# Optimization experiments

Hardware: AMD Instinct MI355X
Metric: run time of the kernel (lower is better)

The kernel has to match this reference:

```python
import jax, jax.numpy as jnp
import numpy as np

B, BS, M, D = 64, 8, 512, 256  # b = bs * neg_sample_num, neg_sample_num = 8
NEG_FILL = -1e10


def setup_inputs() -> dict:
    key = jax.random.key(0)
    ks = jax.random.split(key, 7)
    x = jax.random.normal(ks[0], (B, M, D), jnp.float32)
    y = jax.random.normal(ks[1], (BS, M, D), jnp.float32)
    mask_x = jax.random.randint(ks[2], (B, M), 0, 2).astype(bool).at[:, 0].set(True)
    mask_y = jax.random.randint(ks[3], (BS, M), 0, 2).astype(bool).at[:, 0].set(True)
    scale = 1.0 / np.sqrt(D)
    Wq = jax.random.normal(ks[4], (D, D), jnp.float32) * scale  # torch Linear weight [out,in]
    Wk = jax.random.normal(ks[5], (D, D), jnp.float32) * scale
    Wv = jax.random.normal(ks[6], (D, D), jnp.float32) * scale
    return {"x": x, "y": y, "mask_x": mask_x, "mask_y": mask_y, "Wq": Wq, "Wk": Wk, "Wv": Wv}


def reference(x, y, mask_x, mask_y, Wq, Wk, Wv):
    # Projections (torch Linear: x @ W.T, no bias)
    Qx, Kx, Vx = x @ Wq.T, x @ Wk.T, x @ Wv.T
    Qy, Ky, Vy = y @ Wq.T, y @ Wk.T, y @ Wv.T
    b, m, d = Qx.shape
    bs = Ky.shape[0]
    neg = b // bs  # neg_sample_num branch (bs != b)

    scores_x = jnp.einsum('bid,bjd->bij', Qx, Kx)   # [b,m,m]
    scores_y = jnp.einsum('bid,bjd->bij', Qy, Ky)   # [bs,m,m]
    # Q_x grouped as [bs, neg, m, d] then transposed to [neg, bs, m, d];
    # K_y is tiled over neg (pure broadcast), so contract directly against [bs,m,d].
    Qx_e = Qx.reshape(bs, neg, m, d).swapaxes(0, 1)  # [neg,bs,m,d]
    scores_xy = jnp.einsum('nsid,sjd->nsij', Qx_e, Ky)  # [neg,bs,m,m]

    mx = mask_x[:, :, None]  # [b,m,1]
    my = mask_y[:, :, None]  # [bs,m,1]
    scores_x = jnp.where(mx & mx.swapaxes(1, 2), scores_x, NEG_FILL)
    scores_y = jnp.where(my & my.swapaxes(1, 2), scores_y, NEG_FILL)

    mask_xy = mask_x.reshape(bs, neg, m, 1).swapaxes(0, 1) & mask_y[None, :, None, :]  # [neg,bs,m,m]
    scores_xy = jnp.where(mask_xy, scores_xy, NEG_FILL)

    # y_len[n, s] = sum(mask_y[s]) for every n (repeat/view/sum/transpose in torch)
    y_len = jnp.broadcast_to(jnp.sum(mask_y.astype(jnp.int32), axis=1)[None, :], (neg, bs))

    probs_x = jax.nn.softmax(scores_x, axis=-1)
    probs_y = jax.nn.softmax(scores_y, axis=-1)
    probs_xy = jax.nn.softmax(scores_xy, axis=-1)

    ctx_x = jnp.einsum('bij,bjd->bid', probs_x, Vx)
    ctx_y = jnp.einsum('bij,bjd->bid', probs_y, Vy)
    return (ctx_x, ctx_y, scores_x, scores_y, probs_xy, mask_xy, y_len)
```

## Files before the change

### kernel.cpp

```cpp
#include <hip/hip_runtime.h>
#include <cstdint>

#define NEG_FILL_F (-10000000000.0f)
constexpr int BB     = 64;
constexpr int BS_    = 8;
constexpr int MM     = 512;
constexpr int DD     = 256;
constexpr int ROWS_X = BB * MM;
constexpr int ROWS_Y = BS_ * MM;
constexpr int ROWS_ALL = ROWS_X + ROWS_Y;
constexpr int KS     = 512;

typedef __attribute__((ext_vector_type(8))) short short8;
typedef __attribute__((ext_vector_type(4))) float f32x4;

__device__ inline unsigned short rne_bf16(float f) {
    unsigned int u = __float_as_uint(f);
    u = (u + 0x7FFFu + ((u >> 16) & 1u)) >> 16;
    return (unsigned short)u;
}
__device__ inline float bf2f(unsigned short h) {
    return __uint_as_float(((unsigned int)h) << 16);
}

__device__ inline f32x4 mfma16(short8 a, short8 b, f32x4 c) {
    return __builtin_amdgcn_mfma_f32_16x16x32_bf16(a, b, c, 0, 0, 0);
}

__device__ inline void gld16(const unsigned short* g, unsigned short* l) {
    __builtin_amdgcn_global_load_lds(
        (const __attribute__((address_space(1))) unsigned int*)g,
        (__attribute__((address_space(3))) unsigned int*)l, 16, 0, 0);
}

__device__ inline void mfma_4x4(const short8 af[4], const short8 bf_[4],
                                f32x4 acc[4][4]) {
    #pragma unroll
    for (int i = 0; i < 4; ++i)
        #pragma unroll
        for (int j = 0; j < 4; ++j)
            acc[i][j] = mfma16(af[i], bf_[j], acc[i][j]);
}

__device__ inline int awin32(int w) { return (((w >> 3) == 1) ? 256 : 0) + (w & 7) * 32; }
__device__ inline int bwin32(int w) { return (((w >> 3) == 2) ? 256 : 0) + (w & 7) * 32; }

__device__ inline void stage32(unsigned short* dstbase,
                               const unsigned short* __restrict__ src,
                               int srccol, int wave, int lane)
{
    #pragma unroll
    for (int s4 = 0; s4 < 2; ++s4) {
        const int c   = s4 * 256 + wave * 64 + lane;
        const int r   = c >> 2;
        const int cin = (c & 3) ^ (r & 3);
        gld16(src + (size_t)r * KS + srccol + cin * 8,
              dstbase + (size_t)(s4 * 256 + wave * 64) * 8);
    }
}

__device__ inline void frag4_x32(const unsigned short (*T)[32], int rbase,
                                 int lid, int quad, short8 f[4])
{
    const int q = quad ^ (lid & 3);
    #pragma unroll
    for (int i = 0; i < 4; ++i)
        f[i] = *(const short8*)&T[rbase + i * 16 + lid][q * 8];
}

__global__ __launch_bounds__(256) void convw_kernel(
    const float* __restrict__ Wq, const float* __restrict__ Wk,
    const float* __restrict__ Wv, unsigned short* __restrict__ Wb)
{
    const int g  = blockIdx.x * 256 + threadIdx.x;
    const int e  = g * 8;
    const int zi = e >> 16;
    const int off = e & 65535;
    const int row = off >> 8, k0 = off & 255;
    const float* W = (zi == 0) ? Wq : (zi == 1 ? Wk : Wv);
    float4 v0 = *(const float4*)(W + off);
    float4 v1 = *(const float4*)(W + off + 4);
    const float fv[8] = {v0.x, v0.y, v0.z, v0.w, v1.x, v1.y, v1.z, v1.w};
    short8 hh, ll;
    #pragma unroll
    for (int i = 0; i < 8; ++i) {
        unsigned short h = rne_bf16(fv[i]);
        hh[i] = (short)h;
        ll[i] = (short)rne_bf16(fv[i] - bf2f(h));
    }
    unsigned short* dst = Wb + (size_t)zi * 131072 + (size_t)row * KS;
    *(short8*)(dst + k0)       = hh;
    *(short8*)(dst + 256 + k0) = ll;
}

__global__ __launch_bounds__(256) void convx_kernel(
    const float* __restrict__ x, const float* __restrict__ y,
    unsigned short* __restrict__ xs)
{
    const int g   = blockIdx.x * 256 + threadIdx.x;
    const int row = g >> 5;
    const int off = (g & 31) * 8;
    const float* src = (row < ROWS_X) ? (x + (size_t)row * DD)
                                      : (y + (size_t)(row - ROWS_X) * DD);
    float4 v0 = *(const float4*)(src + off);
    float4 v1 = *(const float4*)(src + off + 4);
    const float fv[8] = {v0.x, v0.y, v0.z, v0.w, v1.x, v1.y, v1.z, v1.w};
    short8 hh, ll;
    #pragma unroll
    for (int i = 0; i < 8; ++i) {
        unsigned short h = rne_bf16(fv[i]);
        hh[i] = (short)h;
        ll[i] = (short)rne_bf16(fv[i] - bf2f(h));
    }
    unsigned short* dst = xs + (size_t)row * KS;
    *(short8*)(dst + off)       = hh;
    *(short8*)(dst + 256 + off) = ll;
}

__global__ __launch_bounds__(256) void proj_kernel(
    const unsigned short* __restrict__ xs,
    const unsigned short* __restrict__ Wb,
    unsigned short* __restrict__ Qa, unsigned short* __restrict__ Kb,
    unsigned short* __restrict__ Vt)
{
    const int xcd = blockIdx.x & 7, idx = blockIdx.x >> 3;
    const int lin = xcd * 216 + idx;
    const int bx  = lin / 6;
    const int rem = lin - bx * 6;
    const int z    = rem >> 1;
    const int row0 = bx * 128;
    const int col0 = (rem & 1) * 128;
    const unsigned short* Asrc = xs + (size_t)row0 * KS;
    const unsigned short* Bsrc = Wb + (size_t)z * 131072 + (size_t)col0 * KS;

    __shared__ unsigned short Ab[2][128][32];
    __shared__ unsigned short Bb[2][128][32];

    const int t = threadIdx.x;
    const int wave = t >> 6, lane = t & 63, quad = lane >> 4, lid = lane & 15;
    const int wrow = (wave & 1) * 64, wcol = (wave >> 1) * 64;

    f32x4 acc[4][4];
    #pragma unroll
    for (int i = 0; i < 4; ++i)
        #pragma unroll
        for (int j = 0; j < 4; ++j) acc[i][j] = (f32x4){0.f, 0.f, 0.f, 0.f};

    stage32(&Ab[0][0][0], Asrc, awin32(0), wave, lane);
    stage32(&Bb[0][0][0], Bsrc, bwin32(0), wave, lane);
    __syncthreads();
    int cur = 0;
    for (int w = 0; w < 23; ++w) {
        stage32(&Ab[cur ^ 1][0][0], Asrc, awin32(w + 1), wave, lane);
        stage32(&Bb[cur ^ 1][0][0], Bsrc, bwin32(w + 1), wave, lane);
        short8 af[4], bf_[4];
        frag4_x32(Ab[cur], wrow, lid, quad, af);
        frag4_x32(Bb[cur], wcol, lid, quad, bf_);
        mfma_4x4(af, bf_, acc);
        __syncthreads();
        cur ^= 1;
    }
    {
        short8 af[4], bf_[4];
        frag4_x32(Ab[cur], wrow, lid, quad, af);
        frag4_x32(Bb[cur], wcol, lid, quad, bf_);
        mfma_4x4(af, bf_, acc);
    }

    if (z == 2) {
        #pragma unroll
        for (int i = 0; i < 4; ++i) {
            const int rg = row0 + wrow + i * 16 + quad * 4;
            const int b  = rg >> 9;
            const int j  = rg & 511;
            #pragma unroll
            for (int jt = 0; jt < 4; ++jt) {
                const int col = col0 + wcol + jt * 16 + lid;
                *(ushort4*)(Vt + (size_t)b * DD * MM + (size_t)col * MM + j) =
                    make_ushort4(rne_bf16(acc[i][jt][0]), rne_bf16(acc[i][jt][1]),
                                 rne_bf16(acc[i][jt][2]), rne_bf16(acc[i][jt][3]));
            }
        }
    } else {
        unsigned short* dst = (z == 0) ? Qa : Kb;
        #pragma unroll
        for (int i = 0; i < 4; ++i) {
            const int rg = row0 + wrow + i * 16 + quad * 4;
            #pragma unroll
            for (int r = 0; r < 4; ++r) {
                unsigned short* rowp = dst + (size_t)(rg + r) * KS;
                #pragma unroll
                for (int jt = 0; jt < 4; ++jt) {
                    const int col = col0 + wcol + jt * 16 + lid;
                    const float v = acc[i][jt][r];
                    unsigned short h = rne_bf16(v);
                    rowp[col]       = h;
                    rowp[256 + col] = rne_bf16(v - bf2f(h));
                }
            }
        }
    }
}

__global__ __launch_bounds__(256) void scores_self_kernel(
    const unsigned short* __restrict__ Qa,
    const unsigned short* __restrict__ Kb,
    const int* __restrict__ mask_x, const int* __restrict__ mask_y,
    float* __restrict__ Sbase, float2* __restrict__ pstats)
{
    const int xcd = blockIdx.x & 7, idx = blockIdx.x >> 3;
    const int lin = xcd * 144 + idx;
    const int z   = lin >> 4;
    const int rem = lin & 15;
    const int row0 = (rem & 3) * 128;
    const int col0 = (rem >> 2) * 128;
    const int by   = rem >> 2;
    const unsigned short* Asrc = Qa + (size_t)(z * MM + row0) * KS;
    const unsigned short* Bsrc = Kb + (size_t)(z * MM + col0) * KS;
    const int* msk = (z < 64) ? (mask_x + z * MM) : (mask_y + (z - 64) * MM);
    float* S = Sbase + (size_t)z * MM * MM;

    __shared__ unsigned short Ab[2][128][32];
    __shared__ unsigned short Bb[2][128][32];
    __shared__ float pm2[128][2];
    __shared__ float ps2[128][2];

    const int t = threadIdx.x;
    const int wave = t >> 6, lane = t & 63, quad = lane >> 4, lid = lane & 15;
    const int wrow = (wave & 1) * 64, wcol = (wave >> 1) * 64;

    f32x4 acc[4][4];
    #pragma unroll
    for (int i = 0; i < 4; ++i)
        #pragma unroll
        for (int j = 0; j < 4; ++j) acc[i][j] = (f32x4){0.f, 0.f, 0.f, 0.f};

    stage32(&Ab[0][0][0], Asrc, awin32(0), wave, lane);
    stage32(&Bb[0][0][0], Bsrc, bwin32(0), wave, lane);
    __syncthreads();
    int cur = 0;
    for (int w = 0; w < 23; ++w) {
        stage32(&Ab[cur ^ 1][0][0], Asrc, awin32(w + 1), wave, lane);
        stage32(&Bb[cur ^ 1][0][0], Bsrc, bwin32(w + 1), wave, lane);
        short8 af[4], bf_[4];
        frag4_x32(Ab[cur], wrow, lid, quad, af);
        frag4_x32(Bb[cur], wcol, lid, quad, bf_);
        mfma_4x4(af, bf_, acc);
        __syncthreads();
        cur ^= 1;
    }
    {
        short8 af[4], bf_[4];
        frag4_x32(Ab[cur], wrow, lid, quad, af);
        frag4_x32(Bb[cur], wcol, lid, quad, bf_);
        mfma_4x4(af, bf_, acc);
    }

    int mcol[4];
    #pragma unroll
    for (int jt = 0; jt < 4; ++jt) mcol[jt] = msk[col0 + wcol + jt * 16 + lid];

    #pragma unroll
    for (int i = 0; i < 4; ++i) {
        const int rl0 = wrow + i * 16 + quad * 4;
        #pragma unroll
        for (int r = 0; r < 4; ++r) {
            const int rlocal = rl0 + r;
            const int rg = row0 + rlocal;
            const bool mr = (msk[rg] != 0);
            float* Srow = S + (size_t)rg * MM;
            float v[4];
            float mt = -3.4e38f;
            #pragma unroll
            for (int jt = 0; jt < 4; ++jt) {
                const int col = col0 + wcol + jt * 16 + lid;
                const bool valid = mr && (mcol[jt] != 0);
                v[jt] = valid ? acc[i][jt][r] : NEG_FILL_F;
                Srow[col] = v[jt];
                mt = fmaxf(mt, v[jt]);
            }
            #pragma unroll
            for (int o = 1; o < 16; o <<= 1) mt = fmaxf(mt, __shfl_xor(mt, o));
            float se = 0.f;
            #pragma unroll
            for (int jt = 0; jt < 4; ++jt) se += __expf(v[jt] - mt);
            #pragma unroll
            for (int o = 1; o < 16; o <<= 1) se += __shfl_xor(se, o);
            if (lid == 0) { pm2[rlocal][wave >> 1] = mt; ps2[rlocal][wave >> 1] = se; }
        }
    }
    __syncthreads();
    if (t < 128) {
        const float m0 = pm2[t][0], m1 = pm2[t][1];
        const float mm = fmaxf(m0, m1);
        const float ss = ps2[t][0] * __expf(m0 - mm) + ps2[t][1] * __expf(m1 - mm);
        pstats[(size_t)(z * 4 + by) * MM + row0 + t] = make_float2(mm, ss);
    }
}

__global__ __launch_bounds__(256) void scores_xy_kernel(
    const unsigned short* __restrict__ Qa, const unsigned short* __restrict__ Kb,
    const int* __restrict__ mask_x, const int* __restrict__ mask_y,
    float* __restrict__ Sbase, float* __restrict__ Mbase,
    float2* __restrict__ pstats)
{
    const int xcd = blockIdx.x & 7, idx = blockIdx.x >> 3;
    const int lin = xcd * 128 + idx;
    const int zz  = lin >> 4;
    const int rem = lin & 15;
    const int s = zz >> 3, n = zz & 7;
    const int zo = n * 8 + s;
    const int bq = s * 8 + n;
    const int bk = s;
    const int row0 = (rem & 3) * 128;
    const int col0 = (rem >> 2) * 128;
    const int by   = rem >> 2;
    const unsigned short* Asrc = Qa + (size_t)(bq * MM + row0) * KS;
    const unsigned short* Bsrc = Kb + (size_t)((ROWS_X + bk * MM) + col0) * KS;
    const int* mq = mask_x + bq * MM;
    const int* mk = mask_y + bk * MM;
    float* Sl = Sbase + (size_t)zo * MM * MM;
    float* Ml = Mbase + (size_t)zo * MM * MM;

    __shared__ unsigned short Ab[2][128][32];
    __shared__ unsigned short Bb[2][128][32];
    __shared__ float pm2[128][2];
    __shared__ float ps2[128][2];

    const int t = threadIdx.x;
    const int wave = t >> 6, lane = t & 63, quad = lane >> 4, lid = lane & 15;
    const int wrow = (wave & 1) * 64, wcol = (wave >> 1) * 64;

    f32x4 acc[4][4];
    #pragma unroll
    for (int i = 0; i < 4; ++i)
        #pragma unroll
        for (int j = 0; j < 4; ++j) acc[i][j] = (f32x4){0.f, 0.f, 0.f, 0.f};

    stage32(&Ab[0][0][0], Asrc, 0, wave, lane);
    stage32(&Bb[0][0][0], Bsrc, 0, wave, lane);
    __syncthreads();
    int cur = 0;
    for (int w = 0; w < 7; ++w) {
        stage32(&Ab[cur ^ 1][0][0], Asrc, (w + 1) * 32, wave, lane);
        stage32(&Bb[cur ^ 1][0][0], Bsrc, (w + 1) * 32, wave, lane);
        short8 af[4], bf_[4];
        frag4_x32(Ab[cur], wrow, lid, quad, af);
        frag4_x32(Bb[cur], wcol, lid, quad, bf_);
        mfma_4x4(af, bf_, acc);
        __syncthreads();
        cur ^= 1;
    }
    {
        short8 af[4], bf_[4];
        frag4_x32(Ab[cur], wrow, lid, quad, af);
        frag4_x32(Bb[cur], wcol, lid, quad, bf_);
        mfma_4x4(af, bf_, acc);
    }

    int mcol[4];
    #pragma unroll
    for (int jt = 0; jt < 4; ++jt) mcol[jt] = mk[col0 + wcol + jt * 16 + lid];

    #pragma unroll
    for (int i = 0; i < 4; ++i) {
        const int rl0 = wrow + i * 16 + quad * 4;
        #pragma unroll
        for (int r = 0; r < 4; ++r) {
            const int rlocal = rl0 + r;
            const int rg = row0 + rlocal;
            const bool mr = (mq[rg] != 0);
            float* Srow = Sl + (size_t)rg * MM;
            float* Mrow = Ml + (size_t)rg * MM;
            float v[4];
            float mt = -3.4e38f;
            #pragma unroll
            for (int jt = 0; jt < 4; ++jt) {
                const int col = col0 + wcol + jt * 16 + lid;
                const bool valid = mr && (mcol[jt] != 0);
                v[jt] = valid ? acc[i][jt][r] : NEG_FILL_F;
                Srow[col] = v[jt];
                Mrow[col] = valid ? 1.0f : 0.0f;
                mt = fmaxf(mt, v[jt]);
            }
            #pragma unroll
            for (int o = 1; o < 16; o <<= 1) mt = fmaxf(mt, __shfl_xor(mt, o));
            float se = 0.f;
            #pragma unroll
            for (int jt = 0; jt < 4; ++jt) se += __expf(v[jt] - mt);
            #pragma unroll
            for (int o = 1; o < 16; o <<= 1) se += __shfl_xor(se, o);
            if (lid == 0) { pm2[rlocal][wave >> 1] = mt; ps2[rlocal][wave >> 1] = se; }
        }
    }
    __syncthreads();
    if (t < 128) {
        const float m0 = pm2[t][0], m1 = pm2[t][1];
        const float mm = fmaxf(m0, m1);
        const float ss = ps2[t][0] * __expf(m0 - mm) + ps2[t][1] * __expf(m1 - mm);
        pstats[(size_t)(zo * 4 + by) * MM + row0 + t] = make_float2(mm, ss);
    }
}

__global__ __launch_bounds__(256) void reduce4_kernel(
    const float2* __restrict__ p, float2* __restrict__ st)
{
    const int row = blockIdx.x * 256 + threadIdx.x;
    const int z = row >> 9, rl = row & 511;
    float m = -3.4e38f, s = 0.f;
    #pragma unroll
    for (int by = 0; by < 4; ++by) {
        float2 v = p[(size_t)(z * 4 + by) * MM + rl];
        float nm = fmaxf(m, v.x);
        s = s * __expf(m - nm) + v.y * __expf(v.x - nm);
        m = nm;
    }
    st[row] = make_float2(m, 1.0f / s);
}

__global__ __launch_bounds__(512) void ctx_kernel(
    const float* __restrict__ Sbase, const float2* __restrict__ stats,
    const unsigned short* __restrict__ Vt_base, float* __restrict__ Obase)
{
    const int xcd = blockIdx.x & 7, idx = blockIdx.x >> 3;
    const int lin = xcd * 36 + idx;
    const int b    = lin >> 2;
    const int row0 = (lin & 3) * 128;
    const float*          S  = Sbase + (size_t)b * MM * MM;
    const float2*         st = stats + (size_t)b * MM;
    const unsigned short* Vt = Vt_base + (size_t)b * DD * MM;
    float*                O  = Obase + (size_t)b * MM * DD;

    __shared__ unsigned short Abuf[2][128][32];
    __shared__ unsigned short Bbuf[2][256][32];

    const int t = threadIdx.x;
    const int wave = t >> 6, lane = t & 63, quad = lane >> 4, lid = lane & 15;
    const int wrow = (wave & 1) * 64, wcol = (wave >> 1) * 64;

    f32x4 acc[4][4];
    #pragma unroll
    for (int i = 0; i < 4; ++i)
        #pragma unroll
        for (int j = 0; j < 4; ++j) acc[i][j] = (f32x4){0.f, 0.f, 0.f, 0.f};

    auto stageB = [&](unsigned short* dstbase, int w) {
        #pragma unroll
        for (int s4 = 0; s4 < 2; ++s4) {
            const int c   = s4 * 512 + wave * 64 + lane;
            const int r   = c >> 2;
            const int cin = (c & 3) ^ (r & 3);
            gld16(Vt + (size_t)r * MM + w * 32 + cin * 8,
                  dstbase + (size_t)(s4 * 512 + wave * 64) * 8);
        }
    };
    auto stageA = [&](unsigned short (*Ab)[32], int w) {
        const int c    = t;
        const int r    = c >> 2;
        const int q    = c & 3;
        const int slot = q ^ (r & 3);
        const float* sp = S + (size_t)(row0 + r) * MM + w * 32 + q * 8;
        float4 v0 = *(const float4*)sp;
        float4 v1 = *(const float4*)(sp + 4);
        const float pm = st[row0 + r].x;
        short8 pk;
        pk[0] = (short)rne_bf16(__expf(v0.x - pm));
        pk[1] = (short)rne_bf16(__expf(v0.y - pm));
        pk[2] = (short)rne_bf16(__expf(v0.z - pm));
        pk[3] = (short)rne_bf16(__expf(v0.w - pm));
        pk[4] = (short)rne_bf16(__expf(v1.x - pm));
        pk[5] = (short)rne_bf16(__expf(v1.y - pm));
        pk[6] = (short)rne_bf16(__expf(v1.z - pm));
        pk[7] = (short)rne_bf16(__expf(v1.w - pm));
        *(short8*)&Ab[r][slot * 8] = pk;
    };

    stageB(&Bbuf[0][0][0], 0);
    stageA(Abuf[0], 0);
    __syncthreads();
    int cur = 0;
    for (int w = 0; w < 15; ++w) {
        stageB(&Bbuf[cur ^ 1][0][0], w + 1);
        stageA(Abuf[cur ^ 1], w + 1);
        short8 af[4], bf_[4];
        frag4_x32(Abuf[cur], wrow, lid, quad, af);
        frag4_x32(Bbuf[cur], wcol, lid, quad, bf_);
        mfma_4x4(af, bf_, acc);
        __syncthreads();
        cur ^= 1;
    }
    {
        short8 af[4], bf_[4];
        frag4_x32(Abuf[cur], wrow, lid, quad, af);
        frag4_x32(Bbuf[cur], wcol, lid, quad, bf_);
        mfma_4x4(af, bf_, acc);
    }

    #pragma unroll
    for (int i = 0; i < 4; ++i) {
        const int rgb = row0 + wrow + i * 16 + quad * 4;
        float inv[4];
        #pragma unroll
        for (int r = 0; r < 4; ++r) inv[r] = st[rgb + r].y;
        #pragma unroll
        for (int jt = 0; jt < 4; ++jt) {
            const int col = wcol + jt * 16 + lid;
            #pragma unroll
            for (int r = 0; r < 4; ++r)
                O[(size_t)(rgb + r) * DD + col] = acc[i][jt][r] * inv[r];
        }
    }
}

__global__ __launch_bounds__(128) void softmax_apply(
    float* __restrict__ S, const float2* __restrict__ ps)
{
    const int row = blockIdx.x;
    const int z = row >> 9, rl = row & 511;
    float m = -3.4e38f, s = 0.f;
    #pragma unroll
    for (int by = 0; by < 4; ++by) {
        float2 v = ps[(size_t)(z * 4 + by) * MM + rl];
        float nm = fmaxf(m, v.x);
        s = s * __expf(m - nm) + v.y * __expf(v.x - nm);
        m = nm;
    }
    const float inv = 1.0f / s;
    float4* r = (float4*)(S + (size_t)row * MM) + threadIdx.x;
    float4 v = *r;
    v.x = __expf(v.x - m) * inv;
    v.y = __expf(v.y - m) * inv;
    v.z = __expf(v.z - m) * inv;
    v.w = __expf(v.w - m) * inv;
    *r = v;
}

__global__ void ylen_kernel(const int* __restrict__ mask_y, float* __restrict__ out)
{
    const int s = blockIdx.x;
    const int lane = threadIdx.x;
    int c = 0;
    #pragma unroll
    for (int k = 0; k < 8; ++k) c += (mask_y[s * MM + k * 64 + lane] != 0);
    #pragma unroll
    for (int off = 32; off; off >>= 1) c += __shfl_xor(c, off);
    if (lane < 8) out[lane * 8 + s] = (float)c;
}

extern "C" void kernel_launch(void* const* d_in, const int* in_sizes, int n_in,
                              void* d_out, int out_size, void* d_ws, size_t ws_size,
                              hipStream_t stream)
{
    const float* x      = (const float*)d_in[0];
    const float* y      = (const float*)d_in[1];
    const int*   mask_x = (const int*)d_in[2];
    const int*   mask_y = (const int*)d_in[3];
    const float* Wq     = (const float*)d_in[4];
    const float* Wk     = (const float*)d_in[5];
    const float* Wv     = (const float*)d_in[6];
    float* out = (float*)d_out;

    unsigned short* Wb = (unsigned short*)d_ws;
    unsigned short* xs = Wb + 393216;
    unsigned short* Qa = xs + 18874368;
    unsigned short* Kb = Qa + 18874368;
    unsigned short* Vt = Kb + 18874368;
    float2* stats_x = (float2*)(Vt + 9437184);
    float2* ps_x    = stats_x + ROWS_ALL;
    float2* ps_xy   = ps_x + 72 * 4 * 512;

    float* out_ctx_x = out;
    float* out_sx    = out + 9437184;
    float* out_pxy   = out + 28311552;
    float* out_mxy   = out + 45088768;
    float* out_ylen  = out + 61865984;

    convw_kernel<<<96, 256, 0, stream>>>(Wq, Wk, Wv, Wb);
    convx_kernel<<<4608, 256, 0, stream>>>(x, y, xs);
    ylen_kernel<<<8, 64, 0, stream>>>(mask_y, out_ylen);

    proj_kernel<<<1728, 256, 0, stream>>>(xs, Wb, Qa, Kb, Vt);

    scores_self_kernel<<<1152, 256, 0, stream>>>(
        Qa, Kb, mask_x, mask_y, out_sx, ps_x);
    scores_xy_kernel<<<1024, 256, 0, stream>>>(
        Qa, Kb, mask_x, mask_y, out_pxy, out_mxy, ps_xy);

    reduce4_kernel<<<ROWS_ALL / 256, 256, 0, stream>>>(ps_x, stats_x);

    softmax_apply<<<ROWS_X, 128, 0, stream>>>(out_pxy, ps_xy);

    ctx_kernel<<<288, 512, 0, stream>>>(out_sx, stats_x, Vt, out_ctx_x);
}
```

Baseline: 485.2 us.

## Compute full-row softmax inside score kernels and stage bf16 probs for ctx

Score kernels now give each block 64 full rows (all 512 columns), so row max and sum are finished inside the block. That removes the partial-stats reduction kernel and the separate softmax_apply pass over probs_xy. The self-score kernel also writes unnormalized bf16 exp values into a scratch P buffer (the probs_xy output region, overwritten later by scores_xy), so ctx_kernel can feed MFMA directly without re-reading fp32 scores and recomputing exp. The cost is a larger LDS footprint (a 512-row B tile), 8x4 accumulator tiles per wave with higher register pressure, an extra bf16 P write and read, and ordering the launches so scores_xy runs after ctx.

```diff
diff --git a/kernel.cpp b/kernel.cpp
--- a/kernel.cpp
+++ b/kernel.cpp
@@ -31,15 +31,6 @@
     __builtin_amdgcn_global_load_lds(
         (const __attribute__((address_space(1))) unsigned int*)g,
         (__attribute__((address_space(3))) unsigned int*)l, 16, 0, 0);
-}
-
-__device__ inline void mfma_4x4(const short8 af[4], const short8 bf_[4],
-                                f32x4 acc[4][4]) {
-    #pragma unroll
-    for (int i = 0; i < 4; ++i)
-        #pragma unroll
-        for (int j = 0; j < 4; ++j)
-            acc[i][j] = mfma16(af[i], bf_[j], acc[i][j]);
 }
 
 __device__ inline int awin32(int w) { return (((w >> 3) == 1) ? 256 : 0) + (w & 7) * 32; }
@@ -156,7 +147,11 @@
         short8 af[4], bf_[4];
         frag4_x32(Ab[cur], wrow, lid, quad, af);
         frag4_x32(Bb[cur], wcol, lid, quad, bf_);
-        mfma_4x4(af, bf_, acc);
+        #pragma unroll
+        for (int i = 0; i < 4; ++i)
+            #pragma unroll
+            for (int j = 0; j < 4; ++j)
+                acc[i][j] = mfma16(af[i], bf_[j], acc[i][j]);
         __syncthreads();
         cur ^= 1;
     }
@@ -164,7 +159,11 @@
         short8 af[4], bf_[4];
         frag4_x32(Ab[cur], wrow, lid, quad, af);
         frag4_x32(Bb[cur], wcol, lid, quad, bf_);
-        mfma_4x4(af, bf_, acc);
+        #pragma unroll
+        for (int i = 0; i < 4; ++i)
+            #pragma unroll
+            for (int j = 0; j < 4; ++j)
+                acc[i][j] = mfma16(af[i], bf_[j], acc[i][j]);
     }
 
     if (z == 2) {
@@ -202,241 +201,286 @@
     }
 }
 
-__global__ __launch_bounds__(256) void scores_self_kernel(
+__global__ __launch_bounds__(256, 2) void scores_self_kernel(
     const unsigned short* __restrict__ Qa,
     const unsigned short* __restrict__ Kb,
     const int* __restrict__ mask_x, const int* __restrict__ mask_y,
-    float* __restrict__ Sbase, float2* __restrict__ pstats)
+    float* __restrict__ Sbase, unsigned short* __restrict__ P,
+    float* __restrict__ inv_all)
 {
     const int xcd = blockIdx.x & 7, idx = blockIdx.x >> 3;
-    const int lin = xcd * 144 + idx;
-    const int z   = lin >> 4;
-    const int rem = lin & 15;
-    const int row0 = (rem & 3) * 128;
-    const int col0 = (rem >> 2) * 128;
-    const int by   = rem >> 2;
-    const unsigned short* Asrc = Qa + (size_t)(z * MM + row0) * KS;
-    const unsigned short* Bsrc = Kb + (size_t)(z * MM + col0) * KS;
+    const int lin = xcd * 72 + idx;
+    const int z    = lin >> 3;
+    const int brow = (lin & 7) * 64;
+    const unsigned short* Asrc = Qa + (size_t)(z * MM + brow) * KS;
+    const unsigned short* Bsrc = Kb + (size_t)z * MM * KS;
     const int* msk = (z < 64) ? (mask_x + z * MM) : (mask_y + (z - 64) * MM);
     float* S = Sbase + (size_t)z * MM * MM;
 
-    __shared__ unsigned short Ab[2][128][32];
-    __shared__ unsigned short Bb[2][128][32];
-    __shared__ float pm2[128][2];
-    __shared__ float ps2[128][2];
+    __shared__ unsigned short Ab[2][64][32];
+    __shared__ unsigned short Bb[2][512][32];
+    __shared__ float pm4[64][4], ps4[64][4], smx[64];
 
     const int t = threadIdx.x;
     const int wave = t >> 6, lane = t & 63, quad = lane >> 4, lid = lane & 15;
-    const int wrow = (wave & 1) * 64, wcol = (wave >> 1) * 64;
-
-    f32x4 acc[4][4];
+    const int wcol = wave * 128;
+
+    f32x4 acc[4][8];
     #pragma unroll
     for (int i = 0; i < 4; ++i)
         #pragma unroll
-        for (int j = 0; j < 4; ++j) acc[i][j] = (f32x4){0.f, 0.f, 0.f, 0.f};
-
-    stage32(&Ab[0][0][0], Asrc, awin32(0), wave, lane);
-    stage32(&Bb[0][0][0], Bsrc, bwin32(0), wave, lane);
+        for (int j = 0; j < 8; ++j) acc[i][j] = (f32x4){0.f, 0.f, 0.f, 0.f};
+
+    auto stage = [&](int buf, int w) {
+        {
+            const int r = t >> 2, cin = (t & 3) ^ (r & 3);
+            gld16(Asrc + (size_t)r * KS + awin32(w) + cin * 8,
+                  &Ab[buf][0][0] + (size_t)(wave * 64) * 8);
+        }
+        const int bw = bwin32(w);
+        #pragma unroll
+        for (int k = 0; k < 8; ++k) {
+            const int c = k * 256 + t;
+            const int r = c >> 2, cin = (c & 3) ^ (r & 3);
+            gld16(Bsrc + (size_t)r * KS + bw + cin * 8,
+                  &Bb[buf][0][0] + (size_t)(k * 256 + wave * 64) * 8);
+        }
+    };
+    auto comp = [&](int buf) {
+        short8 af[4], bv[8];
+        frag4_x32(Ab[buf], 0, lid, quad, af);
+        frag4_x32(Bb[buf], wcol, lid, quad, bv);
+        frag4_x32(Bb[buf], wcol + 64, lid, quad, bv + 4);
+        #pragma unroll
+        for (int i = 0; i < 4; ++i)
+            #pragma unroll
+            for (int j = 0; j < 8; ++j)
+                acc[i][j] = mfma16(af[i], bv[j], acc[i][j]);
+    };
+
+    stage(0, 0);
     __syncthreads();
     int cur = 0;
     for (int w = 0; w < 23; ++w) {
-        stage32(&Ab[cur ^ 1][0][0], Asrc, awin32(w + 1), wave, lane);
-        stage32(&Bb[cur ^ 1][0][0], Bsrc, bwin32(w + 1), wave, lane);
-        short8 af[4], bf_[4];
-        frag4_x32(Ab[cur], wrow, lid, quad, af);
-        frag4_x32(Bb[cur], wcol, lid, quad, bf_);
-        mfma_4x4(af, bf_, acc);
+        stage(cur ^ 1, w + 1);
+        comp(cur);
         __syncthreads();
         cur ^= 1;
     }
-    {
-        short8 af[4], bf_[4];
-        frag4_x32(Ab[cur], wrow, lid, quad, af);
-        frag4_x32(Bb[cur], wcol, lid, quad, bf_);
-        mfma_4x4(af, bf_, acc);
-    }
-
-    int mcol[4];
-    #pragma unroll
-    for (int jt = 0; jt < 4; ++jt) mcol[jt] = msk[col0 + wcol + jt * 16 + lid];
+    comp(cur);
+
+    int mcol[8];
+    #pragma unroll
+    for (int j = 0; j < 8; ++j) mcol[j] = msk[wcol + j * 16 + lid];
 
     #pragma unroll
     for (int i = 0; i < 4; ++i) {
-        const int rl0 = wrow + i * 16 + quad * 4;
         #pragma unroll
         for (int r = 0; r < 4; ++r) {
-            const int rlocal = rl0 + r;
-            const int rg = row0 + rlocal;
-            const bool mr = (msk[rg] != 0);
-            float* Srow = S + (size_t)rg * MM;
-            float v[4];
+            const int rl = i * 16 + quad * 4 + r;
+            const bool mr = (msk[brow + rl] != 0);
+            float* Srow = S + (size_t)(brow + rl) * MM;
+            float vv[8];
             float mt = -3.4e38f;
             #pragma unroll
-            for (int jt = 0; jt < 4; ++jt) {
-                const int col = col0 + wcol + jt * 16 + lid;
-                const bool valid = mr && (mcol[jt] != 0);
-                v[jt] = valid ? acc[i][jt][r] : NEG_FILL_F;
-                Srow[col] = v[jt];
-                mt = fmaxf(mt, v[jt]);
+            for (int j = 0; j < 8; ++j) {
+                const int col = wcol + j * 16 + lid;
+                const bool valid = mr && (mcol[j] != 0);
+                vv[j] = valid ? acc[i][j][r] : NEG_FILL_F;
+                Srow[col] = vv[j];
+                mt = fmaxf(mt, vv[j]);
             }
             #pragma unroll
             for (int o = 1; o < 16; o <<= 1) mt = fmaxf(mt, __shfl_xor(mt, o));
             float se = 0.f;
             #pragma unroll
-            for (int jt = 0; jt < 4; ++jt) se += __expf(v[jt] - mt);
+            for (int j = 0; j < 8; ++j) se += __expf(vv[j] - mt);
             #pragma unroll
             for (int o = 1; o < 16; o <<= 1) se += __shfl_xor(se, o);
-            if (lid == 0) { pm2[rlocal][wave >> 1] = mt; ps2[rlocal][wave >> 1] = se; }
-        }
-    }
-    __syncthreads();
-    if (t < 128) {
-        const float m0 = pm2[t][0], m1 = pm2[t][1];
-        const float mm = fmaxf(m0, m1);
-        const float ss = ps2[t][0] * __expf(m0 - mm) + ps2[t][1] * __expf(m1 - mm);
-        pstats[(size_t)(z * 4 + by) * MM + row0 + t] = make_float2(mm, ss);
-    }
-}
-
-__global__ __launch_bounds__(256) void scores_xy_kernel(
+            if (lid == 0) { pm4[rl][wave] = mt; ps4[rl][wave] = se; }
+        }
+    }
+    __syncthreads();
+    if (t < 64) {
+        const float m = fmaxf(fmaxf(pm4[t][0], pm4[t][1]),
+                              fmaxf(pm4[t][2], pm4[t][3]));
+        float s = 0.f;
+        #pragma unroll
+        for (int c = 0; c < 4; ++c) s += ps4[t][c] * __expf(pm4[t][c] - m);
+        smx[t] = m;
+        inv_all[z * MM + brow + t] = 1.0f / s;
+    }
+    __syncthreads();
+    #pragma unroll
+    for (int i = 0; i < 4; ++i) {
+        #pragma unroll
+        for (int r = 0; r < 4; ++r) {
+            const int rl = i * 16 + quad * 4 + r;
+            const bool mr = (msk[brow + rl] != 0);
+            const float m = smx[rl];
+            unsigned short* Prow = P + (size_t)(z * MM + brow + rl) * KS;
+            #pragma unroll
+            for (int j = 0; j < 8; ++j) {
+                const int col = wcol + j * 16 + lid;
+                const bool valid = mr && (mcol[j] != 0);
+                const float v = valid ? acc[i][j][r] : NEG_FILL_F;
+                Prow[col] = rne_bf16(__expf(v - m));
+            }
+        }
+    }
+}
+
+__global__ __launch_bounds__(256, 2) void scores_xy_kernel(
     const unsigned short* __restrict__ Qa, const unsigned short* __restrict__ Kb,
     const int* __restrict__ mask_x, const int* __restrict__ mask_y,
-    float* __restrict__ Sbase, float* __restrict__ Mbase,
-    float2* __restrict__ pstats)
+    float* __restrict__ Prb, float* __restrict__ Mb)
 {
     const int xcd = blockIdx.x & 7, idx = blockIdx.x >> 3;
-    const int lin = xcd * 128 + idx;
-    const int zz  = lin >> 4;
-    const int rem = lin & 15;
+    const int lin = xcd * 64 + idx;
+    const int zz = lin >> 3;
+    const int brow = (lin & 7) * 64;
     const int s = zz >> 3, n = zz & 7;
     const int zo = n * 8 + s;
     const int bq = s * 8 + n;
     const int bk = s;
-    const int row0 = (rem & 3) * 128;
-    const int col0 = (rem >> 2) * 128;
-    const int by   = rem >> 2;
-    const unsigned short* Asrc = Qa + (size_t)(bq * MM + row0) * KS;
-    const unsigned short* Bsrc = Kb + (size_t)((ROWS_X + bk * MM) + col0) * KS;
+    const unsigned short* Asrc = Qa + (size_t)(bq * MM + brow) * KS;
+    const unsigned short* Bsrc = Kb + (size_t)(ROWS_X + bk * MM) * KS;
     const int* mq = mask_x + bq * MM;
     const int* mk = mask_y + bk * MM;
-    float* Sl = Sbase + (size_t)zo * MM * MM;
-    float* Ml = Mbase + (size_t)zo * MM * MM;
-
-    __shared__ unsigned short Ab[2][128][32];
-    __shared__ unsigned short Bb[2][128][32];
-    __shared__ float pm2[128][2];
-    __shared__ float ps2[128][2];
+    float* Pl = Prb + (size_t)zo * MM * MM;
+    float* Ml = Mb  + (size_t)zo * MM * MM;
+
+    __shared__ unsigned short Ab[2][64][32];
+    __shared__ unsigned short Bb[2][512][32];
+    __shared__ float pm4[64][4], ps4[64][4], smx[64], sin[64];
 
     const int t = threadIdx.x;
     const int wave = t >> 6, lane = t & 63, quad = lane >> 4, lid = lane & 15;
-    const int wrow = (wave & 1) * 64, wcol = (wave >> 1) * 64;
-
-    f32x4 acc[4][4];
+    const int wcol = wave * 128;
+
+    f32x4 acc[4][8];
     #pragma unroll
     for (int i = 0; i < 4; ++i)
         #pragma unroll
-        for (int j = 0; j < 4; ++j) acc[i][j] = (f32x4){0.f, 0.f, 0.f, 0.f};
-
-    stage32(&Ab[0][0][0], Asrc, 0, wave, lane);
-    stage32(&Bb[0][0][0], Bsrc, 0, wave, lane);
+        for (int j = 0; j < 8; ++j) acc[i][j] = (f32x4){0.f, 0.f, 0.f, 0.f};
+
+    auto stage = [&](int buf, int w) {
+        {
+            const int r = t >> 2, cin = (t & 3) ^ (r & 3);
+            gld16(Asrc + (size_t)r * KS + w * 32 + cin * 8,
+                  &Ab[buf][0][0] + (size_t)(wave * 64) * 8);
+        }
+        #pragma unroll
+        for (int k = 0; k < 8; ++k) {
+            const int c = k * 256 + t;
+            const int r = c >> 2, cin = (c & 3) ^ (r & 3);
+            gld16(Bsrc + (size_t)r * KS + w * 32 + cin * 8,
+                  &Bb[buf][0][0] + (size_t)(k * 256 + wave * 64) * 8);
+        }
+    };
+    auto comp = [&](int buf) {
+        short8 af[4], bv[8];
+        frag4_x32(Ab[buf], 0, lid, quad, af);
+        frag4_x32(Bb[buf], wcol, lid, quad, bv);
+        frag4_x32(Bb[buf], wcol + 64, lid, quad, bv + 4);
+        #pragma unroll
+        for (int i = 0; i < 4; ++i)
+            #pragma unroll
+            for (int j = 0; j < 8; ++j)
+                acc[i][j] = mfma16(af[i], bv[j], acc[i][j]);
+    };
+
+    stage(0, 0);
     __syncthreads();
     int cur = 0;
     for (int w = 0; w < 7; ++w) {
-        stage32(&Ab[cur ^ 1][0][0], Asrc, (w + 1) * 32, wave, lane);
-        stage32(&Bb[cur ^ 1][0][0], Bsrc, (w + 1) * 32, wave, lane);
-        short8 af[4], bf_[4];
-        frag4_x32(Ab[cur], wrow, lid, quad, af);
-        frag4_x32(Bb[cur], wcol, lid, quad, bf_);
-        mfma_4x4(af, bf_, acc);
+        stage(cur ^ 1, w + 1);
+        comp(cur);
         __syncthreads();
         cur ^= 1;
     }
-    {
-        short8 af[4], bf_[4];
-        frag4_x32(Ab[cur], wrow, lid, quad, af);
-        frag4_x32(Bb[cur], wcol, lid, quad, bf_);
-        mfma_4x4(af, bf_, acc);
-    }
-
-    int mcol[4];
-    #pragma unroll
-    for (int jt = 0; jt < 4; ++jt) mcol[jt] = mk[col0 + wcol + jt * 16 + lid];
+    comp(cur);
+
+    int mcol[8];
+    #pragma unroll
+    for (int j = 0; j < 8; ++j) mcol[j] = mk[wcol + j * 16 + lid];
 
     #pragma unroll
     for (int i = 0; i < 4; ++i) {
-        const int rl0 = wrow + i * 16 + quad * 4;
         #pragma unroll
         for (int r = 0; r < 4; ++r) {
-            const int rlocal = rl0 + r;
-            const int rg = row0 + rlocal;
-            const bool mr = (mq[rg] != 0);
-            float* Srow = Sl + (size_t)rg * MM;
-            float* Mrow = Ml + (size_t)rg * MM;
-            float v[4];
+            const int rl = i * 16 + quad * 4 + r;
+            const bool mr = (mq[brow + rl] != 0);
+            float* Mrow = Ml + (size_t)(brow + rl) * MM;
+            float vv[8];
             float mt = -3.4e38f;
             #pragma unroll
-            for (int jt = 0; jt < 4; ++jt) {
-                const int col = col0 + wcol + jt * 16 + lid;
-                const bool valid = mr && (mcol[jt] != 0);
-                v[jt] = valid ? acc[i][jt][r] : NEG_FILL_F;
-                Srow[col] = v[jt];
+            for (int j = 0; j < 8; ++j) {
+                const int col = wcol + j * 16 + lid;
+                const bool valid = mr && (mcol[j] != 0);
+                vv[j] = valid ? acc[i][j][r] : NEG_FILL_F;
                 Mrow[col] = valid ? 1.0f : 0.0f;
-                mt = fmaxf(mt, v[jt]);
+                mt = fmaxf(mt, vv[j]);
             }
             #pragma unroll
             for (int o = 1; o < 16; o <<= 1) mt = fmaxf(mt, __shfl_xor(mt, o));
             float se = 0.f;
             #pragma unroll
-            for (int jt = 0; jt < 4; ++jt) se += __expf(v[jt] - mt);
+            for (int j = 0; j < 8; ++j) se += __expf(vv[j] - mt);
             #pragma unroll
             for (int o = 1; o < 16; o <<= 1) se += __shfl_xor(se, o);
-            if (lid == 0) { pm2[rlocal][wave >> 1] = mt; ps2[rlocal][wave >> 1] = se; }
-        }
-    }
-    __syncthreads();
-    if (t < 128) {
-        const float m0 = pm2[t][0], m1 = pm2[t][1];
-        const float mm = fmaxf(m0, m1);
-        const float ss = ps2[t][0] * __expf(m0 - mm) + ps2[t][1] * __expf(m1 - mm);
-        pstats[(size_t)(zo * 4 + by) * MM + row0 + t] = make_float2(mm, ss);
-    }
-}
-
-__global__ __launch_bounds__(256) void reduce4_kernel(
-    const float2* __restrict__ p, float2* __restrict__ st)
-{
-    const int row = blockIdx.x * 256 + threadIdx.x;
-    const int z = row >> 9, rl = row & 511;
-    float m = -3.4e38f, s = 0.f;
-    #pragma unroll
-    for (int by = 0; by < 4; ++by) {
-        float2 v = p[(size_t)(z * 4 + by) * MM + rl];
-        float nm = fmaxf(m, v.x);
-        s = s * __expf(m - nm) + v.y * __expf(v.x - nm);
-        m = nm;
-    }
-    st[row] = make_float2(m, 1.0f / s);
-}
-
-__global__ __launch_bounds__(512) void ctx_kernel(
-    const float* __restrict__ Sbase, const float2* __restrict__ stats,
+            if (lid == 0) { pm4[rl][wave] = mt; ps4[rl][wave] = se; }
+        }
+    }
+    __syncthreads();
+    if (t < 64) {
+        const float m = fmaxf(fmaxf(pm4[t][0], pm4[t][1]),
+                              fmaxf(pm4[t][2], pm4[t][3]));
+        float ssum = 0.f;
+        #pragma unroll
+        for (int c = 0; c < 4; ++c) ssum += ps4[t][c] * __expf(pm4[t][c] - m);
+        smx[t] = m;
+        sin[t] = 1.0f / ssum;
+    }
+    __syncthreads();
+    #pragma unroll
+    for (int i = 0; i < 4; ++i) {
+        #pragma unroll
+        for (int r = 0; r < 4; ++r) {
+            const int rl = i * 16 + quad * 4 + r;
+            const bool mr = (mq[brow + rl] != 0);
+            const float m = smx[rl], iv = sin[rl];
+            float* Prow = Pl + (size_t)(brow + rl) * MM;
+            #pragma unroll
+            for (int j = 0; j < 8; ++j) {
+                const int col = wcol + j * 16 + lid;
+                const bool valid = mr && (mcol[j] != 0);
+                const float v = valid ? acc[i][j][r] : NEG_FILL_F;
+                Prow[col] = __expf(v - m) * iv;
+            }
+        }
+    }
+}
+
+__global__ __launch_bounds__(256) void ctx_kernel(
+    const unsigned short* __restrict__ P, const float* __restrict__ inv_all,
     const unsigned short* __restrict__ Vt_base, float* __restrict__ Obase)
 {
     const int xcd = blockIdx.x & 7, idx = blockIdx.x >> 3;
-    const int lin = xcd * 36 + idx;
-    const int b    = lin >> 2;
-    const int row0 = (lin & 3) * 128;
-    const float*          S  = Sbase + (size_t)b * MM * MM;
-    const float2*         st = stats + (size_t)b * MM;
-    const unsigned short* Vt = Vt_base + (size_t)b * DD * MM;
-    float*                O  = Obase + (size_t)b * MM * DD;
-
-    __shared__ unsigned short Abuf[2][128][32];
-    __shared__ unsigned short Bbuf[2][256][32];
+    const int lin = xcd * 72 + idx;
+    const int b    = lin >> 3;
+    const int brow = (lin & 7) * 64;
+    const unsigned short* Psrc = P + (size_t)(b * MM + brow) * KS;
+    const unsigned short* Vt   = Vt_base + (size_t)b * DD * MM;
+    float*                O    = Obase + (size_t)b * MM * DD;
+    const float*          iv   = inv_all + b * MM + brow;
+
+    __shared__ unsigned short Ab[2][64][32];
+    __shared__ unsigned short Bb[2][256][32];
 
     const int t = threadIdx.x;
     const int wave = t >> 6, lane = t & 63, quad = lane >> 4, lid = lane & 15;
-    const int wrow = (wave & 1) * 64, wcol = (wave >> 1) * 64;
+    const int wcol = wave * 64;
 
     f32x4 acc[4][4];
     #pragma unroll
@@ -444,95 +488,56 @@
         #pragma unroll
         for (int j = 0; j < 4; ++j) acc[i][j] = (f32x4){0.f, 0.f, 0.f, 0.f};
 
-    auto stageB = [&](unsigned short* dstbase, int w) {
-        #pragma unroll
-        for (int s4 = 0; s4 < 2; ++s4) {
-            const int c   = s4 * 512 + wave * 64 + lane;
-            const int r   = c >> 2;
-            const int cin = (c & 3) ^ (r & 3);
+    auto stage = [&](int buf, int w) {
+        {
+            const int r = t >> 2, cin = (t & 3) ^ (r & 3);
+            gld16(Psrc + (size_t)r * KS + w * 32 + cin * 8,
+                  &Ab[buf][0][0] + (size_t)(wave * 64) * 8);
+        }
+        #pragma unroll
+        for (int k = 0; k < 4; ++k) {
+            const int c = k * 256 + t;
+            const int r = c >> 2, cin = (c & 3) ^ (r & 3);
             gld16(Vt + (size_t)r * MM + w * 32 + cin * 8,
-                  dstbase + (size_t)(s4 * 512 + wave * 64) * 8);
+                  &Bb[buf][0][0] + (size_t)(k * 256 + wave * 64) * 8);
         }
     };
-    auto stageA = [&](unsigned short (*Ab)[32], int w) {
-        const int c    = t;
-        const int r    = c >> 2;
-        const int q    = c & 3;
-        const int slot = q ^ (r & 3);
-        const float* sp = S + (size_t)(row0 + r) * MM + w * 32 + q * 8;
-        float4 v0 = *(const float4*)sp;
-        float4 v1 = *(const float4*)(sp + 4);
-        const float pm = st[row0 + r].x;
-        short8 pk;
-        pk[0] = (short)rne_bf16(__expf(v0.x - pm));
-        pk[1] = (short)rne_bf16(__expf(v0.y - pm));
-        pk[2] = (short)rne_bf16(__expf(v0.z - pm));
-        pk[3] = (short)rne_bf16(__expf(v0.w - pm));
-        pk[4] = (short)rne_bf16(__expf(v1.x - pm));
-        pk[5] = (short)rne_bf16(__expf(v1.y - pm));
-        pk[6] = (short)rne_bf16(__expf(v1.z - pm));
-        pk[7] = (short)rne_bf16(__expf(v1.w - pm));
-        *(short8*)&Ab[r][slot * 8] = pk;
+    auto comp = [&](int buf) {
+        short8 af[4], bf_[4];
+        frag4_x32(Ab[buf], 0, lid, quad, af);
+        frag4_x32(Bb[buf], wcol, lid, quad, bf_);
+        #pragma unroll
+        for (int i = 0; i < 4; ++i)
+            #pragma unroll
+            for (int j = 0; j < 4; ++j)
+                acc[i][j] = mfma16(af[i], bf_[j], acc[i][j]);
     };
 
-    stageB(&Bbuf[0][0][0], 0);
-    stageA(Abuf[0], 0);
+    stage(0, 0);
     __syncthreads();
     int cur = 0;
     for (int w = 0; w < 15; ++w) {
-        stageB(&Bbuf[cur ^ 1][0][0], w + 1);
-        stageA(Abuf[cur ^ 1], w + 1);
-        short8 af[4], bf_[4];
-        frag4_x32(Abuf[cur], wrow, lid, quad, af);
-        frag4_x32(Bbuf[cur], wcol, lid, quad, bf_);
-        mfma_4x4(af, bf_, acc);
+        stage(cur ^ 1, w + 1);
+        comp(cur);
         __syncthreads();
         cur ^= 1;
     }
-    {
-        short8 af[4], bf_[4];
-        frag4_x32(Abuf[cur], wrow, lid, quad, af);
-        frag4_x32(Bbuf[cur], wcol, lid, quad, bf_);
-        mfma_4x4(af, bf_, acc);
-    }
+    comp(cur);
 
     #pragma unroll
     for (int i = 0; i < 4; ++i) {
-        const int rgb = row0 + wrow + i * 16 + quad * 4;
+        const int rl0 = i * 16 + quad * 4;
         float inv[4];
         #pragma unroll
-        for (int r = 0; r < 4; ++r) inv[r] = st[rgb + r].y;
+        for (int r = 0; r < 4; ++r) inv[r] = iv[rl0 + r];
         #pragma unroll
         for (int jt = 0; jt < 4; ++jt) {
             const int col = wcol + jt * 16 + lid;
             #pragma unroll
             for (int r = 0; r < 4; ++r)
-                O[(size_t)(rgb + r) * DD + col] = acc[i][jt][r] * inv[r];
-        }
-    }
-}
-
-__global__ __launch_bounds__(128) void softmax_apply(
-    float* __restrict__ S, const float2* __restrict__ ps)
-{
-    const int row = blockIdx.x;
-    const int z = row >> 9, rl = row & 511;
-    float m = -3.4e38f, s = 0.f;
-    #pragma unroll
-    for (int by = 0; by < 4; ++by) {
-        float2 v = ps[(size_t)(z * 4 + by) * MM + rl];
-        float nm = fmaxf(m, v.x);
-        s = s * __expf(m - nm) + v.y * __expf(v.x - nm);
-        m = nm;
-    }
-    const float inv = 1.0f / s;
-    float4* r = (float4*)(S + (size_t)row * MM) + threadIdx.x;
-    float4 v = *r;
-    v.x = __expf(v.x - m) * inv;
-    v.y = __expf(v.y - m) * inv;
-    v.z = __expf(v.z - m) * inv;
-    v.w = __expf(v.w - m) * inv;
-    *r = v;
+                O[(size_t)(brow + rl0 + r) * DD + col] = acc[i][jt][r] * inv[r];
+        }
+    }
 }
 
 __global__ void ylen_kernel(const int* __restrict__ mask_y, float* __restrict__ out)
@@ -565,30 +570,27 @@
     unsigned short* Qa = xs + 18874368;
     unsigned short* Kb = Qa + 18874368;
     unsigned short* Vt = Kb + 18874368;
-    float2* stats_x = (float2*)(Vt + 9437184);
-    float2* ps_x    = stats_x + ROWS_ALL;
-    float2* ps_xy   = ps_x + 72 * 4 * 512;
-
-    float* out_ctx_x = out;
+    float* inv_all = (float*)(Vt + 9437184);
+
+    float* out_ctx   = out;
     float* out_sx    = out + 9437184;
     float* out_pxy   = out + 28311552;
     float* out_mxy   = out + 45088768;
     float* out_ylen  = out + 61865984;
 
+    unsigned short* P = (unsigned short*)out_pxy;
+
     convw_kernel<<<96, 256, 0, stream>>>(Wq, Wk, Wv, Wb);
     convx_kernel<<<4608, 256, 0, stream>>>(x, y, xs);
     ylen_kernel<<<8, 64, 0, stream>>>(mask_y, out_ylen);
 
     proj_kernel<<<1728, 256, 0, stream>>>(xs, Wb, Qa, Kb, Vt);
 
-    scores_self_kernel<<<1152, 256, 0, stream>>>(
-        Qa, Kb, mask_x, mask_y, out_sx, ps_x);
-    scores_xy_kernel<<<1024, 256, 0, stream>>>(
-        Qa, Kb, mask_x, mask_y, out_pxy, out_mxy, ps_xy);
-
-    reduce4_kernel<<<ROWS_ALL / 256, 256, 0, stream>>>(ps_x, stats_x);
-
-    softmax_apply<<<ROWS_X, 128, 0, stream>>>(out_pxy, ps_xy);
-
-    ctx_kernel<<<288, 512, 0, stream>>>(out_sx, stats_x, Vt, out_ctx_x);
-}
+    scores_self_kernel<<<576, 256, 0, stream>>>(
+        Qa, Kb, mask_x, mask_y, out_sx, P, inv_all);
+
+    ctx_kernel<<<576, 256, 0, stream>>>(P, inv_all, Vt, out_ctx);
+
+    scores_xy_kernel<<<512, 256, 0, stream>>>(
+        Qa, Kb, mask_x, mask_y, out_pxy, out_mxy);
+}
```

Measured after the change: 465.1 us. -4.1%, faster.
